# Kernel tuning notes

Hardware: AMD Instinct MI355X
Metric: run time of the kernel (lower is better)

## Reference

```python
import jax, jax.numpy as jnp
import numpy as np

ITERATIONS = 100  # resonator iterations (default in __init__)


def _quantize(x):
    # MAP/bipolar quantize: sign with ties -> +1
    return jnp.where(x >= 0, 1.0, -1.0).astype(x.dtype)


def _resonator_step(inp, estimates, codebooks):
    # inp: (b, d); estimates: (b, f, d); codebooks: (f, v, d)
    f = estimates.shape[-2]
    # rolled copies, stacked: (b, f, f-1, d); product = multibind of all other factors
    rolled = jnp.stack([jnp.roll(estimates, i, axis=-3 + 1) for i in range(1, f)], axis=-2)
    inv_others = jnp.prod(rolled, axis=-2)              # (b, f, d)
    new_estimates = inp[:, None, :] * inv_others        # bind, (b, f, d)
    similarity = jnp.einsum('bfd,fvd->bfv', new_estimates, codebooks)  # (b, f, v)
    # multiset with similarity weights, then quantize
    output = _quantize(jnp.einsum('bfv,fvd->bfd', similarity, codebooks))
    max_sim = jnp.max(similarity, axis=-1)              # (b, f)
    return output, max_sim


def setup_inputs() -> dict:
    key = jax.random.key(0)
    b, f, v, d = 1024, 4, 64, 2048
    k1, k2 = jax.random.split(key)
    # bipolar codebooks (f, v, d)
    codebooks = _quantize(jax.random.normal(k1, (f, v, d), dtype=jnp.float32))
    # construct a solvable input: bind of one random codevector per factor
    idx = jax.random.randint(k2, (b, f), 0, v)          # (b, f)
    chosen = codebooks[jnp.arange(f)[None, :], idx]     # (b, f, d)
    inp = jnp.prod(chosen, axis=1)                      # (b, d)
    # init estimates: quantized multiset (bundle) of each codebook, tiled over batch
    init = _quantize(jnp.sum(codebooks, axis=1))        # (f, d)
    init_estimates = jnp.broadcast_to(init[None], (b, f, d)).astype(jnp.float32)
    return {"input": inp, "init_estimates": init_estimates, "codebooks": codebooks}


def reference(input, init_estimates, codebooks):
    # Concurrent resonator network, fixed iteration count (data-dependent
    # early-convergence check omitted for jit compatibility).
    def body(est, _):
        out, max_sim = _resonator_step(input, est, codebooks)
        return out, max_sim

    estimates, max_sims = jax.lax.scan(body, init_estimates, None, length=ITERATIONS)
    # cleanup: argmax of |similarity| against codebooks (argmax_abs=True)
    sim = jnp.einsum('bfd,fvd->bfv', estimates, codebooks)
    outcome = jnp.argmax(jnp.abs(sim), axis=-1).astype(jnp.int32)  # (b, f)
    convergence = jnp.int32(ITERATIONS - 1)
    return estimates, outcome, max_sims[-1], convergence
```

## Files before the change

### kernel.cpp

```cpp
#include <hip/hip_runtime.h>
#include <stdint.h>


#define NB 1024
#define NF 4
#define ND 2048
#define NW 32
#define ITERS 100
#define NRB 4

#define OFF_OUT  (NB*NF*ND)
#define OFF_MS   (OFF_OUT + NB*NF)
#define OFF_CONV (OFF_MS + NB*NF)

typedef unsigned long long u64;

__global__ void pack_cb_kernel(const float* __restrict__ cb,
                               u64* __restrict__ cbB, u64* __restrict__ cbT) {
    const int lane = threadIdx.x & 63;
    const int gw   = (blockIdx.x * (blockDim.x >> 6)) + (threadIdx.x >> 6);
    const int nw   = (gridDim.x * blockDim.x) >> 6;
    for (int idx = gw; idx < NF * 64 * NW; idx += nw) {
        const int j = idx >> 11, v = (idx >> 5) & 63, w = idx & 31;
        const float x = cb[(((j << 6) | v) << 11) + (w << 6) + lane];
        const u64 m = __ballot(x < 0.0f);
        if (lane == 0)
            cbB[(((((j << 4) | (w >> 1)) << 6) | v) << 1) | (w & 1)] = m;
    }
    for (int idx = gw; idx < NF * ND; idx += nw) {
        const int j = idx >> 11, d = idx & 2047;
        const float x = cb[(((j << 6) | lane) << 11) + d];
        const u64 m = __ballot(x < 0.0f);
        const int w = d >> 6, la = d & 63;
        if (lane == 0)
            cbT[(((((j << 4) | (w >> 1)) << 6) | la) << 1) | (w & 1)] = m;
    }
}

#define PCW(CW, W)                                                           \
    {                                                                        \
        const u64 cw_ = (CW);                                                \
        int t = base + cmul * (int)__popcll(cw_);                            \
        t += (int)__popcll(c0 & cw_) << 2;                                   \
        t += (int)__popcll(c1 & cw_) << 3;                                   \
        t += (int)__popcll(c2 & cw_) << 4;                                   \
        t += (int)__popcll(c3 & cw_) << 5;                                   \
        t += (int)__popcll(c4 & cw_) << 6;                                   \
        t += (int)__popcll(c5 & cw_) << 7;                                   \
        t += (int)__popcll(c6 & cw_) << 8;                                   \
        t += (int)__popcll(c7 & cw_) << 9;                                   \
        t += oe0 * (int)((cw_ >> ov0) & 1);                                  \
        t += oe1 * (int)((cw_ >> ov1) & 1);                                  \
        if (nov > 2) {                              \
            u64 m2 = om;                                                     \
            while (m2) {                                                     \
                const int vv = __builtin_ctzll(m2); m2 &= m2 - 1;            \
                t += 4 * __builtin_amdgcn_readlane(ex, vv)                   \
                       * (int)((cw_ >> vv) & 1);                             \
            }                                                                \
        }                                                                    \
        const u64 nww = __ballot(t < 0);                                     \
        if (lane == 0) s_hist[r][nxt][j][W] = nww;                           \
    }

__global__ __launch_bounds__(1024, 2) void resonator_kernel(
    const float* __restrict__ inp, const float* __restrict__ est_init,
    const u64* __restrict__ cbB, const u64* __restrict__ cbT,
    float* __restrict__ out) {
    __shared__ u64 l_cbB[NF * 16 * 64 * 2];
    __shared__ u64 l_cbT[NF * 16 * 64 * 2];
    __shared__ u64 s_hist[NRB][3][NF][NW];
    __shared__ u64 s_inp[NRB][NW];
    __shared__ u64 s_ne[NRB][NF][NW];
    __shared__ int s_conv[NRB][NF];
    __shared__ int s_fs[NRB];

    const int b    = blockIdx.x;
    const int tid  = threadIdx.x;
    const int wid  = tid >> 6;
    const int lane = tid & 63;
    const int j    = wid & 3;
    const int r    = wid >> 2;
    const int row  = (b << 2) + r;

    for (int idx = tid; idx < NF * 16 * 64 * 2; idx += 1024) {
        l_cbB[idx] = cbB[idx];
        l_cbT[idx] = cbT[idx];
    }
    #pragma unroll
    for (int k = 0; k < 8; ++k) {
        const int w = (j << 3) + k;
        const u64 m = __ballot(inp[(row << 11) + (w << 6) + lane] < 0.0f);
        if (lane == 0) s_inp[r][w] = m;
    }
    #pragma unroll 4
    for (int w = 0; w < NW; ++w) {
        const u64 m = __ballot(
            est_init[(((row << 2) | j) << 11) + (w << 6) + lane] < 0.0f);
        if (lane == 0) s_hist[r][0][j][w] = m;
    }
    __syncthreads();

    const ulonglong2* tB = (const ulonglong2*)l_cbB + (j << 10) + lane;
    const ulonglong2* tT = (const ulonglong2*)l_cbT + (j << 10) + lane;

    int s100 = -1, s99 = -1;
    int cur = 0, nxt = 1, prv = 2;

    for (int it = 0; it < ITERS; ++it) {
        if (lane < NW) {
            const u64 X = s_inp[r][lane]
                ^ s_hist[r][cur][0][lane] ^ s_hist[r][cur][1][lane]
                ^ s_hist[r][cur][2][lane] ^ s_hist[r][cur][3][lane];
            s_ne[r][j][lane] = X ^ s_hist[r][cur][j][lane];
        }

        int pc = 0;
        #pragma unroll
        for (int hh = 0; hh < 2; ++hh) {
            ulonglong2 gB[8];
            #pragma unroll
            for (int k = 0; k < 8; ++k)
                gB[k] = tB[((hh << 3) | k) << 6];
            #pragma unroll
            for (int k = 0; k < 8; ++k) {
                const int w2 = (hh << 3) | k;
                const ulonglong2 nn =
                    *(const ulonglong2*)&s_ne[r][j][w2 << 1];
                pc += (int)__popcll(nn.x ^ gB[k].x)
                    + (int)__popcll(nn.y ^ gB[k].y);
            }
        }
        int sp = pc;
        #pragma unroll
        for (int off = 32; off > 0; off >>= 1) sp += __shfl_xor(sp, off);

        const int mean = sp >> 6;
        const int dev  = pc - mean;
        const int devc = dev < -128 ? -128 : (dev > 127 ? 127 : dev);
        const int ex   = dev - devc;
        const int u    = devc + 128;
        const u64 c0 = __ballot(u & 1),  c1 = __ballot(u & 2);
        const u64 c2 = __ballot(u & 4),  c3 = __ballot(u & 8);
        const u64 c4 = __ballot(u & 16), c5 = __ballot(u & 32);
        const u64 c6 = __ballot(u & 64), c7 = __ballot(u & 128);
        u64 om = __ballot(ex != 0);
        const int nov = (int)__popcll(om);
        int ov0 = 0, ov1 = 0, oe0 = 0, oe1 = 0;
        if (nov > 0) {
            ov0 = __builtin_ctzll(om); om &= om - 1;
            oe0 = 4 * __builtin_amdgcn_readlane(ex, ov0);
            if (nov > 1) {
                ov1 = __builtin_ctzll(om); om &= om - 1;
                oe1 = 4 * __builtin_amdgcn_readlane(ex, ov1);
            }
        }
        const int base = 131072 - 2 * sp;
        const int cmul = 4 * mean - 4608;

        #pragma unroll
        for (int hh = 0; hh < 2; ++hh) {
            ulonglong2 gT[8];
            #pragma unroll
            for (int k = 0; k < 8; ++k)
                gT[k] = tT[((hh << 3) | k) << 6];
            #pragma unroll
            for (int k = 0; k < 8; ++k) {
                const int w2 = (hh << 3) | k;
                PCW(gT[k].x, (w2 << 1))
                PCW(gT[k].y, (w2 << 1) + 1)
            }
        }

        int d1 = 0, d2 = 0;
        if (lane < NW) {
            const u64 a = s_hist[r][nxt][j][lane];
            d1 = (a != s_hist[r][cur][j][lane]);
            d2 = (a != s_hist[r][prv][j][lane]);
        }
        const u64 b1 = __ballot(d1), b2 = __ballot(d2);
        if (lane == 0) s_conv[r][j] = (b1 == 0 ? 1 : 0) | (b2 == 0 ? 2 : 0);
        __syncthreads();

        int flr = 0;
        bool allok = true;
        #pragma unroll
        for (int r2 = 0; r2 < NRB; ++r2) {
            const int f = s_conv[r2][0] & s_conv[r2][1]
                        & s_conv[r2][2] & s_conv[r2][3];
            if (r2 == r) flr = f;
            allok = allok && ((f & 1) || (it >= 1 && (f & 2)));
        }
        if (allok) {
            if (flr & 1) { s100 = nxt; s99 = nxt; }
            else {
                s100 = (((ITERS - it) & 1) == 0) ? cur : nxt;
                s99  = (s100 == nxt) ? cur : nxt;
            }
            break;
        }
        const int t3 = prv; prv = cur; cur = nxt; nxt = t3;
    }
    if (s100 < 0) { s100 = cur; s99 = prv; }

    if (j == 0 && lane == 0) s_fs[r] = s100;

    int pcO = 0;
    #pragma unroll
    for (int w2 = 0; w2 < 16; ++w2) {
        const ulonglong2 g  = tB[w2 << 6];
        const ulonglong2 hh = *(const ulonglong2*)&s_hist[r][s100][j][w2 << 1];
        pcO += (int)__popcll(hh.x ^ g.x) + (int)__popcll(hh.y ^ g.y);
    }
    const int simF = ND - (pcO << 1);
    const int aF   = simF < 0 ? -simF : simF;
    int key = (aF << 6) | (63 - lane);
    #pragma unroll
    for (int off = 32; off > 0; off >>= 1) {
        const int t1 = __shfl_xor(key, off);
        key = key > t1 ? key : t1;
    }

    int pc9 = 0;
    #pragma unroll
    for (int w2 = 0; w2 < 16; ++w2) {
        const ulonglong2 g = tB[w2 << 6];
        const int w = w2 << 1;
        const u64 X0 = s_inp[r][w]
            ^ s_hist[r][s99][0][w] ^ s_hist[r][s99][1][w]
            ^ s_hist[r][s99][2][w] ^ s_hist[r][s99][3][w];
        const u64 n0 = X0 ^ s_hist[r][s99][j][w];
        const u64 X1 = s_inp[r][w + 1]
            ^ s_hist[r][s99][0][w + 1] ^ s_hist[r][s99][1][w + 1]
            ^ s_hist[r][s99][2][w + 1] ^ s_hist[r][s99][3][w + 1];
        const u64 n1 = X1 ^ s_hist[r][s99][j][w + 1];
        pc9 += (int)__popcll(n0 ^ g.x) + (int)__popcll(n1 ^ g.y);
    }
    int mn9 = pc9;
    #pragma unroll
    for (int off = 32; off > 0; off >>= 1) {
        const int a1 = __shfl_xor(mn9, off);
        mn9 = mn9 < a1 ? mn9 : a1;
    }
    if (lane == 0) {
        out[OFF_OUT + (row << 2) + j] = (float)(63 - (key & 63));
        out[OFF_MS  + (row << 2) + j] = (float)(ND - 2 * mn9);
    }
    __syncthreads();

    #pragma unroll
    for (int rr = 0; rr < NRB; ++rr) {
        const int f2 = s_fs[rr];
        #pragma unroll
        for (int k = 0; k < 8; ++k) {
            const int idx = tid + (k << 10);
            const int jj = idx >> 11, d = idx & 2047;
            const u64 wrd = s_hist[rr][f2][jj][d >> 6];
            out[(((b << 2) + rr) << 13) + idx] =
                ((wrd >> (d & 63)) & 1) ? -1.0f : 1.0f;
        }
    }
    if (b == 0 && tid == 0) out[OFF_CONV] = 99.0f;
}

extern "C" void kernel_launch(void* const* d_in, const int* in_sizes, int n_in,
                              void* d_out, int out_size, void* d_ws, size_t ws_size,
                              hipStream_t stream) {
    const float* inp  = (const float*)d_in[0];
    const float* est0 = (const float*)d_in[1];
    const float* cb   = (const float*)d_in[2];
    float* out = (float*)d_out;
    u64* cbB = (u64*)d_ws;
    u64* cbT = cbB + NF * 16 * 64 * 2;

    pack_cb_kernel<<<64, 256, 0, stream>>>(cb, cbB, cbT);
    resonator_kernel<<<NB / NRB, 1024, 0, stream>>>(inp, est0, cbB, cbT, out);
}
```

Baseline: 1.632 ms.

## Replace block-wide barrier with per-row LDS semaphore and per-row convergence exit

Swaps the per-iteration __syncthreads across all 16 waves for a per-row shared-memory counter that only the 4 waves of one row spin on. Each row can now exit independently once it converges, instead of waiting for all rows in the block. The convergence flags are double-buffered by iteration parity, and the final output write is done per row by each wave, which removes the closing barrier. It also swaps a few multiplies for mul24 and selects. The spin-wait relies on LDS visibility ordering and adds polling overhead per iteration.

```diff
diff --git a/kernel.cpp b/kernel.cpp
--- a/kernel.cpp
+++ b/kernel.cpp
@@ -40,7 +40,7 @@
 #define PCW(CW, W)                                                           \
     {                                                                        \
         const u64 cw_ = (CW);                                                \
-        int t = base + cmul * (int)__popcll(cw_);                            \
+        int t = base + __mul24(cmul, (int)__popcll(cw_));                    \
         t += (int)__popcll(c0 & cw_) << 2;                                   \
         t += (int)__popcll(c1 & cw_) << 3;                                   \
         t += (int)__popcll(c2 & cw_) << 4;                                   \
@@ -49,8 +49,8 @@
         t += (int)__popcll(c5 & cw_) << 7;                                   \
         t += (int)__popcll(c6 & cw_) << 8;                                   \
         t += (int)__popcll(c7 & cw_) << 9;                                   \
-        t += oe0 * (int)((cw_ >> ov0) & 1);                                  \
-        t += oe1 * (int)((cw_ >> ov1) & 1);                                  \
+        t += ((cw_ >> ov0) & 1) ? oe0 : 0;                                   \
+        t += ((cw_ >> ov1) & 1) ? oe1 : 0;                                   \
         if (nov > 2) {                              \
             u64 m2 = om;                                                     \
             while (m2) {                                                     \
@@ -72,8 +72,8 @@
     __shared__ u64 s_hist[NRB][3][NF][NW];
     __shared__ u64 s_inp[NRB][NW];
     __shared__ u64 s_ne[NRB][NF][NW];
-    __shared__ int s_conv[NRB][NF];
-    __shared__ int s_fs[NRB];
+    __shared__ int s_conv[2][NRB][NF];
+    __shared__ int s_sem[NRB];
 
     const int b    = blockIdx.x;
     const int tid  = threadIdx.x;
@@ -87,6 +87,7 @@
         l_cbB[idx] = cbB[idx];
         l_cbT[idx] = cbT[idx];
     }
+    if (tid < NRB) s_sem[tid] = 0;
     #pragma unroll
     for (int k = 0; k < 8; ++k) {
         const int w = (j << 3) + k;
@@ -103,6 +104,7 @@
 
     const ulonglong2* tB = (const ulonglong2*)l_cbB + (j << 10) + lane;
     const ulonglong2* tT = (const ulonglong2*)l_cbT + (j << 10) + lane;
+    volatile int* vsem = (volatile int*)&s_sem[r];
 
     int s100 = -1, s99 = -1;
     int cur = 0, nxt = 1, prv = 2;
@@ -179,19 +181,19 @@
             d2 = (a != s_hist[r][prv][j][lane]);
         }
         const u64 b1 = __ballot(d1), b2 = __ballot(d2);
-        if (lane == 0) s_conv[r][j] = (b1 == 0 ? 1 : 0) | (b2 == 0 ? 2 : 0);
-        __syncthreads();
-
-        int flr = 0;
-        bool allok = true;
-        #pragma unroll
-        for (int r2 = 0; r2 < NRB; ++r2) {
-            const int f = s_conv[r2][0] & s_conv[r2][1]
-                        & s_conv[r2][2] & s_conv[r2][3];
-            if (r2 == r) flr = f;
-            allok = allok && ((f & 1) || (it >= 1 && (f & 2)));
-        }
-        if (allok) {
+        if (lane == 0)
+            s_conv[it & 1][r][j] = (b1 == 0 ? 1 : 0) | (b2 == 0 ? 2 : 0);
+
+        __threadfence_block();
+        if (lane == 0) atomicAdd(&s_sem[r], 1);
+        const int tgt = (it + 1) << 2;
+        while (*vsem < tgt) __builtin_amdgcn_s_sleep(1);
+        __threadfence_block();
+
+        const int p = it & 1;
+        const int flr = s_conv[p][r][0] & s_conv[p][r][1]
+                      & s_conv[p][r][2] & s_conv[p][r][3];
+        if ((flr & 1) || (it >= 1 && (flr & 2))) {
             if (flr & 1) { s100 = nxt; s99 = nxt; }
             else {
                 s100 = (((ITERS - it) & 1) == 0) ? cur : nxt;
@@ -202,8 +204,6 @@
         const int t3 = prv; prv = cur; cur = nxt; nxt = t3;
     }
     if (s100 < 0) { s100 = cur; s99 = prv; }
-
-    if (j == 0 && lane == 0) s_fs[r] = s100;
 
     int pcO = 0;
     #pragma unroll
@@ -246,19 +246,12 @@
         out[OFF_OUT + (row << 2) + j] = (float)(63 - (key & 63));
         out[OFF_MS  + (row << 2) + j] = (float)(ND - 2 * mn9);
     }
-    __syncthreads();
-
-    #pragma unroll
-    for (int rr = 0; rr < NRB; ++rr) {
-        const int f2 = s_fs[rr];
-        #pragma unroll
-        for (int k = 0; k < 8; ++k) {
-            const int idx = tid + (k << 10);
-            const int jj = idx >> 11, d = idx & 2047;
-            const u64 wrd = s_hist[rr][f2][jj][d >> 6];
-            out[(((b << 2) + rr) << 13) + idx] =
-                ((wrd >> (d & 63)) & 1) ? -1.0f : 1.0f;
-        }
+
+    #pragma unroll 4
+    for (int k = 0; k < NW; ++k) {
+        const u64 wrd = s_hist[r][s100][j][k];
+        out[(row << 13) + (j << 11) + (k << 6) + lane] =
+            ((wrd >> lane) & 1) ? -1.0f : 1.0f;
     }
     if (b == 0 && tid == 0) out[OFF_CONV] = 99.0f;
 }
```

New measurement: 1.627 ms. About the same (-0.3%).
